# Kernel optimization log

Measured on AMD Instinct MI355X. Metric: run time of the kernel, lower is better.

The kernel has to match this reference:

```python
import jax, jax.numpy as jnp
import numpy as np

B, F, S, P, E, H = 64, 32, 512, 96, 8, 2048
TOP_K = 2
ALPHA = 10.0
ENT_EPS = 1e-8
CV_EPS = 1e-10


def setup_inputs() -> dict:
    key = jax.random.key(0)
    ks = jax.random.split(key, 8)
    s = 0.02
    return {
        "x": jax.random.normal(ks[0], (B, F, S), dtype=jnp.float32),
        "time_embedding": jax.random.normal(ks[1], (B, F, S), dtype=jnp.float32),
        "Wg": jax.random.normal(ks[2], (S, E), dtype=jnp.float32) * s,
        "bg": jnp.zeros((E,), dtype=jnp.float32),
        "W1": jax.random.normal(ks[3], (E, S, H), dtype=jnp.float32) * s,
        "b1": jnp.zeros((E, H), dtype=jnp.float32),
        "W2": jax.random.normal(ks[4], (E, H, P), dtype=jnp.float32) * s,
        "b2": jnp.zeros((E, P), dtype=jnp.float32),
    }


def _gates(tf, Wg, bg):
    # tf: [F, B, S] -> logits [F, B, E]
    logits = jnp.einsum('fbs,se->fbe', tf, Wg) + bg
    # kthvalue(x, E - top_k + 1) = (E - top_k)-th entry (0-based) of ascending sort = k-th largest
    kth = jnp.sort(logits, axis=-1)[..., E - TOP_K]  # [F, B]
    mask = logits < kth[..., None]
    sm = jax.nn.softmax(logits, axis=-1)
    dec = jnp.where(mask, ALPHA * jnp.log(sm + 1.0), ALPHA * (jnp.exp(sm) - 1.0))
    return jax.nn.softmax(dec, axis=-1)  # [F, B, E]


def reference(x, time_embedding, Wg, bg, W1, b1, W2, b2):
    xf = jnp.transpose(x, (1, 0, 2))               # [F, B, S]
    tf = jnp.transpose(time_embedding, (1, 0, 2))  # [F, B, S]
    gates = _gates(tf, Wg, bg)                     # [F, B, E]

    # all experts on all features (eval mode: dropout = identity)
    h = jax.nn.gelu(jnp.einsum('fbs,esh->febh', xf, W1) + b1[None, :, None, :], approximate=False)
    eo = jnp.einsum('febh,ehp->febp', h, W2) + b2[None, :, None, :]  # [F, E, B, P]
    out = jnp.einsum('fbe,febp->fbp', gates, eo)   # gated weighted sum
    output = jnp.transpose(out, (1, 0, 2))         # [B, F, P]

    # selector loss: cv_squared of importance = gates.sum(batch) expanded over pred_len
    gsum = gates.sum(axis=1)                       # [F, E]
    imp = jnp.broadcast_to(gsum[..., None], (F, E, P)).reshape(F, E * P)
    cv = jnp.var(imp, axis=1, ddof=1) / (jnp.mean(imp, axis=1) ** 2 + CV_EPS)
    selector_loss = jnp.sum(cv)                    # loss_coef = 1.0

    # entropy loss: importance1 = gates.mean(batch) expanded over pred_len
    gmean = gates.mean(axis=1)                     # [F, E]
    imp1 = jnp.broadcast_to(gmean[..., None], (F, E, P))
    entropy_loss = jnp.sum((-imp1 * jnp.log(imp1 + ENT_EPS)).mean(axis=(1, 2)))

    return output, selector_loss, entropy_loss
```

## Files before the change

### kernel.cpp

```cpp
#include <hip/hip_runtime.h>
#include <math.h>

#define B_ 64
#define F_ 32
#define S_ 512
#define P_ 96
#define E_ 8
#define H_ 2048
#define M_ 2048

#define BM 128
#define BH 128
#define BK 64
#define HGROUPS 4
#define HPG (H_ / HGROUPS)
#define NHC (HPG / BH)
#define NKC (S_ / BK)

#define XPITCH 72
#define W1PITCH 72
#define HPITCH 136
#define W2PITCH 136

typedef __bf16 bf16x8 __attribute__((ext_vector_type(8)));
typedef float f32x4 __attribute__((ext_vector_type(4)));
typedef unsigned int u32x4 __attribute__((ext_vector_type(4)));
typedef unsigned int u32x2 __attribute__((ext_vector_type(2)));

#define MFMA16(a, b, c) __builtin_amdgcn_mfma_f32_16x16x32_bf16((a), (b), (c), 0, 0, 0)

__device__ __forceinline__ unsigned short f2bf(float f) {
  unsigned int u = __float_as_uint(f);
  return (unsigned short)((u + 0x7FFFu + ((u >> 16) & 1u)) >> 16);
}

__global__ __launch_bounds__(256) void k_convert_x(const float* __restrict__ x,
                                                   unsigned short* __restrict__ xbf) {
  int i = (blockIdx.x * 256 + threadIdx.x) * 4;
  f32x4 v = *(const f32x4*)(x + i);
  unsigned int lo = (unsigned int)f2bf(v[0]) | ((unsigned int)f2bf(v[1]) << 16);
  unsigned int hi = (unsigned int)f2bf(v[2]) | ((unsigned int)f2bf(v[3]) << 16);
  u32x2 o = {lo, hi};
  *(u32x2*)(xbf + i) = o;
}

template <int R, int C>
__global__ __launch_bounds__(256) void k_transpose(const float* __restrict__ in,
                                                   unsigned short* __restrict__ outbf) {
  __shared__ float tile[32][33];
  int e = blockIdx.z;
  const float* src = in + (size_t)e * R * C;
  unsigned short* dst = outbf + (size_t)e * R * C;
  int c0 = blockIdx.x * 32, r0 = blockIdx.y * 32;
  int tx = threadIdx.x & 31, ty = threadIdx.x >> 5;
#pragma unroll
  for (int i = 0; i < 4; ++i) {
    int r = ty * 4 + i;
    tile[r][tx] = src[(size_t)(r0 + r) * C + c0 + tx];
  }
  __syncthreads();
#pragma unroll
  for (int i = 0; i < 4; ++i) {
    int c = ty * 4 + i;
    dst[(size_t)(c0 + c) * R + r0 + tx] = f2bf(tile[tx][c]);
  }
}

__global__ __launch_bounds__(256) void k_gates(const float* __restrict__ te,
                                               const float* __restrict__ Wg,
                                               const float* __restrict__ bg,
                                               float* __restrict__ gates) {
  int wave = threadIdx.x >> 6;
  int lane = threadIdx.x & 63;
  int m = blockIdx.x * 4 + wave;
  const float* trow = te + (size_t)m * S_;
  float acc[E_];
#pragma unroll
  for (int e = 0; e < E_; ++e) acc[e] = 0.f;
  for (int s = lane; s < S_; s += 64) {
    float t = trow[s];
    const f32x4* wgr = (const f32x4*)(Wg + s * E_);
    f32x4 a = wgr[0], b = wgr[1];
    acc[0] += t * a[0]; acc[1] += t * a[1]; acc[2] += t * a[2]; acc[3] += t * a[3];
    acc[4] += t * b[0]; acc[5] += t * b[1]; acc[6] += t * b[2]; acc[7] += t * b[3];
  }
#pragma unroll
  for (int e = 0; e < E_; ++e) {
#pragma unroll
    for (int off = 32; off > 0; off >>= 1) acc[e] += __shfl_xor(acc[e], off, 64);
  }
  if (lane == 0) {
    float lg[E_];
    float m1 = -3.4e38f, m2 = -3.4e38f;
#pragma unroll
    for (int e = 0; e < E_; ++e) {
      float v = acc[e] + bg[e];
      lg[e] = v;
      if (v > m1) { m2 = m1; m1 = v; }
      else if (v > m2) { m2 = v; }
    }
    float den = 0.f, sm[E_];
#pragma unroll
    for (int e = 0; e < E_; ++e) { sm[e] = expf(lg[e] - m1); den += sm[e]; }
    float inv = 1.f / den;
    float dmax = -3.4e38f, dec[E_];
#pragma unroll
    for (int e = 0; e < E_; ++e) {
      float p = sm[e] * inv;
      float d = (lg[e] < m2) ? (10.f * logf(p + 1.f)) : (10.f * (expf(p) - 1.f));
      dec[e] = d;
      dmax = fmaxf(dmax, d);
    }
    float dden = 0.f;
#pragma unroll
    for (int e = 0; e < E_; ++e) { dec[e] = expf(dec[e] - dmax); dden += dec[e]; }
    float dinv = 1.f / dden;
#pragma unroll
    for (int e = 0; e < E_; ++e) gates[m * E_ + e] = dec[e] * dinv;
  }
}

__global__ __launch_bounds__(256) void k_loss(const float* __restrict__ gates,
                                              float* __restrict__ lout) {
  __shared__ float gsum[F_][E_];
  __shared__ float cvs[F_], ents[F_];
  int t = threadIdx.x;
  int f = t >> 3, e = t & 7;
  float s = 0.f;
  for (int b = 0; b < B_; ++b) s += gates[(size_t)(b * F_ + f) * E_ + e];
  gsum[f][e] = s;
  __syncthreads();
  if (t < F_) {
    float mean = 0.f;
#pragma unroll
    for (int k = 0; k < E_; ++k) mean += gsum[t][k];
    mean *= (1.f / E_);
    float ss = 0.f;
#pragma unroll
    for (int k = 0; k < E_; ++k) { float d = gsum[t][k] - mean; ss += d * d; }
    float var = (float)P_ * ss / (float)(E_ * P_ - 1);
    cvs[t] = var / (mean * mean + 1e-10f);
    float ent = 0.f;
#pragma unroll
    for (int k = 0; k < E_; ++k) { float g = gsum[t][k] * (1.f / B_); ent += -g * logf(g + 1e-8f); }
    ents[t] = ent * (1.f / E_);
  }
  __syncthreads();
  if (t == 0) {
    float a = 0.f, b = 0.f;
    for (int k = 0; k < F_; ++k) { a += cvs[k]; b += ents[k]; }
    lout[0] = a;
    lout[1] = b;
  }
}

__global__ __launch_bounds__(256, 2) void k_experts(
    const unsigned short* __restrict__ xbf,
    const unsigned short* __restrict__ w1t,
    const unsigned short* __restrict__ w2t,
    const float* __restrict__ b1,
    const float* __restrict__ b2,
    const float* __restrict__ gates,
    float* __restrict__ out)
{
  __shared__ __align__(16) unsigned short Xks[BM * XPITCH];
  __shared__ __align__(16) unsigned short Hs[BM * HPITCH];
  __shared__ __align__(16) unsigned short Ws[P_ * W2PITCH];

  const int tid = threadIdx.x;
  const int wave = tid >> 6, lane = tid & 63;
  const int l15 = lane & 15, quad = lane >> 4;
  const int e = blockIdx.x;
  const int m0 = blockIdx.y * BM;
  const int hbase = blockIdx.z * HPG;

  const unsigned short* __restrict__ w1e = w1t + ((size_t)e * H_ + hbase) * S_;
  const unsigned short* __restrict__ w2e = w2t + (size_t)e * P_ * H_ + hbase;
  const float* __restrict__ b1e = b1 + e * H_ + hbase;

  const int rw = (wave >> 1) * 64;
  const int cw = (wave & 1) * 64;

  const int srow = tid >> 3;
  const int scol = (tid & 7) * 8;
  const int trow = tid >> 4;
  const int tcol = (tid & 15) * 8;

  const f32x4 fz = {0.f, 0.f, 0.f, 0.f};
  f32x4 acc2[2][6];
#pragma unroll
  for (int rt = 0; rt < 2; ++rt)
#pragma unroll
    for (int j = 0; j < 6; ++j) acc2[rt][j] = fz;

  for (int hc = 0; hc < NHC; ++hc) {
    f32x4 acc1[4][4];
#pragma unroll
    for (int i = 0; i < 4; ++i)
#pragma unroll
      for (int j = 0; j < 4; ++j) acc1[i][j] = fz;

    u32x4 xreg[4], w1reg[4];
#pragma unroll
    for (int p = 0; p < 4; ++p) {
      int rr = p * 32 + srow;
      xreg[p]  = *(const u32x4*)(xbf + (size_t)(m0 + rr) * S_ + scol);
      w1reg[p] = *(const u32x4*)(w1e + (size_t)(hc * BH + rr) * S_ + scol);
    }
    for (int kc = 0; kc < NKC; ++kc) {
      __syncthreads();
#pragma unroll
      for (int p = 0; p < 4; ++p) {
        int rr = p * 32 + srow;
        *(u32x4*)&Xks[rr * XPITCH + scol] = xreg[p];
        *(u32x4*)&Ws[rr * W1PITCH + scol] = w1reg[p];
      }
      __syncthreads();
      if (kc + 1 < NKC) {
#pragma unroll
        for (int p = 0; p < 4; ++p) {
          int rr = p * 32 + srow;
          xreg[p]  = *(const u32x4*)(xbf + (size_t)(m0 + rr) * S_ + (kc + 1) * BK + scol);
          w1reg[p] = *(const u32x4*)(w1e + (size_t)(hc * BH + rr) * S_ + (kc + 1) * BK + scol);
        }
      }
#pragma unroll
      for (int kk = 0; kk < 2; ++kk) {
        bf16x8 af[4], bfr[4];
#pragma unroll
        for (int i = 0; i < 4; ++i)
          af[i] = *(const bf16x8*)&Xks[(rw + i * 16 + l15) * XPITCH + kk * 32 + quad * 8];
#pragma unroll
        for (int j = 0; j < 4; ++j)
          bfr[j] = *(const bf16x8*)&Ws[(cw + j * 16 + l15) * W1PITCH + kk * 32 + quad * 8];
#pragma unroll
        for (int i = 0; i < 4; ++i)
#pragma unroll
          for (int j = 0; j < 4; ++j)
            acc1[i][j] = MFMA16(af[i], bfr[j], acc1[i][j]);
      }
    }
    u32x4 w2reg[6];
#pragma unroll
    for (int p = 0; p < 6; ++p) {
      int rr = p * 16 + trow;
      w2reg[p] = *(const u32x4*)(w2e + (size_t)rr * H_ + hc * BH + tcol);
    }
#pragma unroll
    for (int j = 0; j < 4; ++j) {
      int n = hc * BH + cw + j * 16 + l15;
      float bias = b1e[n];
#pragma unroll
      for (int i = 0; i < 4; ++i) {
#pragma unroll
        for (int r = 0; r < 4; ++r) {
          float xv = acc1[i][j][r] + bias;
          float g = 0.5f * xv * (1.0f + erff(xv * 0.70710678118654752f));
          Hs[(rw + i * 16 + quad * 4 + r) * HPITCH + cw + j * 16 + l15] = f2bf(g);
        }
      }
    }
    __syncthreads();
#pragma unroll
    for (int p = 0; p < 6; ++p) {
      int rr = p * 16 + trow;
      *(u32x4*)&Ws[rr * W2PITCH + tcol] = w2reg[p];
    }
    __syncthreads();
#pragma unroll
    for (int kk = 0; kk < 4; ++kk) {
      bf16x8 a0 = *(const bf16x8*)&Hs[(wave * 32 + l15) * HPITCH + kk * 32 + quad * 8];
      bf16x8 a1 = *(const bf16x8*)&Hs[(wave * 32 + 16 + l15) * HPITCH + kk * 32 + quad * 8];
#pragma unroll
      for (int j = 0; j < 6; ++j) {
        bf16x8 b = *(const bf16x8*)&Ws[(j * 16 + l15) * W2PITCH + kk * 32 + quad * 8];
        acc2[0][j] = MFMA16(a0, b, acc2[0][j]);
        acc2[1][j] = MFMA16(a1, b, acc2[1][j]);
      }
    }
  }
#pragma unroll
  for (int rt = 0; rt < 2; ++rt) {
#pragma unroll
    for (int r = 0; r < 4; ++r) {
      int m = m0 + wave * 32 + rt * 16 + quad * 4 + r;
      float g = gates[m * E_ + e];
#pragma unroll
      for (int j = 0; j < 6; ++j) {
        int col = j * 16 + l15;
        float v = acc2[rt][j][r];
        if (blockIdx.z == 0) v += b2[e * P_ + col];
        atomicAdd(&out[(size_t)m * P_ + col], g * v);
      }
    }
  }
}

extern "C" void kernel_launch(void* const* d_in, const int* in_sizes, int n_in,
                              void* d_out, int out_size, void* d_ws, size_t ws_size,
                              hipStream_t stream) {
  const float* x  = (const float*)d_in[0];
  const float* te = (const float*)d_in[1];
  const float* Wg = (const float*)d_in[2];
  const float* bg = (const float*)d_in[3];
  const float* W1 = (const float*)d_in[4];
  const float* b1 = (const float*)d_in[5];
  const float* W2 = (const float*)d_in[6];
  const float* b2 = (const float*)d_in[7];
  float* out = (float*)d_out;

  char* ws = (char*)d_ws;
  float* gates        = (float*)ws;
  unsigned short* xbf = (unsigned short*)(ws + 65536);
  unsigned short* w1t = (unsigned short*)(ws + 65536 + 2097152);
  unsigned short* w2t = (unsigned short*)(ws + 65536 + 2097152 + 16777216);

  hipMemsetAsync(d_out, 0, (size_t)out_size * sizeof(float), stream);
  k_convert_x<<<(M_ * S_) / 1024, 256, 0, stream>>>(x, xbf);
  k_transpose<S_, H_><<<dim3(H_ / 32, S_ / 32, E_), 256, 0, stream>>>(W1, w1t);
  k_transpose<H_, P_><<<dim3(P_ / 32, H_ / 32, E_), 256, 0, stream>>>(W2, w2t);
  k_gates<<<M_ / 4, 256, 0, stream>>>(te, Wg, bg, gates);
  k_loss<<<1, 256, 0, stream>>>(gates, out + (size_t)M_ * P_);
  k_experts<<<dim3(E_, M_ / BM, HGROUPS), 256, 0, stream>>>(xbf, w1t, w2t, b1, b2, gates, out);
}
```

Baseline: 203.8 us.

## Fuse prep kernels, fold loss into experts, double-buffer W1 and read X/W2 from global

Merges the x conversion, both weight transposes and the gate computation into one k_prep launch, and moves the loss reduction into an extra z-slice of the expert kernel, cutting the launch count from six to two plus the memset. Inside the expert GEMM, W1 tiles are double-buffered in LDS with one barrier per k-step, while X and W2 fragments are loaded straight from global memory into registers. Exact erf GELU is replaced by a sigmoid-based approximation built on exp2 and rcp intrinsics, and the H store is vectorized. The GELU approximation changes numerics and could exceed tolerance. The direct global fragment loads depend on cache hits for their latency.

New measurement: 269.5 us. 32.2% more time.

```diff
diff --git a/kernel.cpp b/kernel.cpp
--- a/kernel.cpp
+++ b/kernel.cpp
@@ -17,62 +17,90 @@
 #define NHC (HPG / BH)
 #define NKC (S_ / BK)
 
-#define XPITCH 72
 #define W1PITCH 72
-#define HPITCH 136
-#define W2PITCH 136
+#define HPITCH 132
 
 typedef __bf16 bf16x8 __attribute__((ext_vector_type(8)));
+typedef __bf16 bf16x4 __attribute__((ext_vector_type(4)));
 typedef float f32x4 __attribute__((ext_vector_type(4)));
 typedef unsigned int u32x4 __attribute__((ext_vector_type(4)));
-typedef unsigned int u32x2 __attribute__((ext_vector_type(2)));
 
 #define MFMA16(a, b, c) __builtin_amdgcn_mfma_f32_16x16x32_bf16((a), (b), (c), 0, 0, 0)
 
-__device__ __forceinline__ unsigned short f2bf(float f) {
-  unsigned int u = __float_as_uint(f);
-  return (unsigned short)((u + 0x7FFFu + ((u >> 16) & 1u)) >> 16);
-}
-
-__global__ __launch_bounds__(256) void k_convert_x(const float* __restrict__ x,
-                                                   unsigned short* __restrict__ xbf) {
-  int i = (blockIdx.x * 256 + threadIdx.x) * 4;
-  f32x4 v = *(const f32x4*)(x + i);
-  unsigned int lo = (unsigned int)f2bf(v[0]) | ((unsigned int)f2bf(v[1]) << 16);
-  unsigned int hi = (unsigned int)f2bf(v[2]) | ((unsigned int)f2bf(v[3]) << 16);
-  u32x2 o = {lo, hi};
-  *(u32x2*)(xbf + i) = o;
-}
-
-template <int R, int C>
-__global__ __launch_bounds__(256) void k_transpose(const float* __restrict__ in,
-                                                   unsigned short* __restrict__ outbf) {
-  __shared__ float tile[32][33];
-  int e = blockIdx.z;
-  const float* src = in + (size_t)e * R * C;
-  unsigned short* dst = outbf + (size_t)e * R * C;
-  int c0 = blockIdx.x * 32, r0 = blockIdx.y * 32;
-  int tx = threadIdx.x & 31, ty = threadIdx.x >> 5;
-#pragma unroll
-  for (int i = 0; i < 4; ++i) {
-    int r = ty * 4 + i;
-    tile[r][tx] = src[(size_t)(r0 + r) * C + c0 + tx];
+__device__ __forceinline__ float fast_gelu(float x) {
+  float e = __builtin_amdgcn_exp2f(-2.45546696f * x);
+  return x * __builtin_amdgcn_rcpf(1.0f + e);
+}
+
+#define PREP_GRID 4096
+
+__device__ __forceinline__ void transpose_tile(const float* __restrict__ src,
+                                               __bf16* __restrict__ dst,
+                                               int R, int C, int r0, int c0, int cw,
+                                               float* tile ) {
+  const int tid = threadIdx.x;
+  {
+    int row = tid >> 2;
+    int cseg = (tid & 3) * 16;
+    const float* s = src + (size_t)(r0 + row) * C + c0;
+#pragma unroll
+    for (int k = 0; k < 4; ++k) {
+      int c = cseg + k * 4;
+      if (c < cw) *(f32x4*)&tile[row * 68 + c] = *(const f32x4*)(s + c);
+    }
   }
   __syncthreads();
-#pragma unroll
-  for (int i = 0; i < 4; ++i) {
-    int c = ty * 4 + i;
-    dst[(size_t)(c0 + c) * R + r0 + tx] = f2bf(tile[tx][c]);
-  }
-}
-
-__global__ __launch_bounds__(256) void k_gates(const float* __restrict__ te,
-                                               const float* __restrict__ Wg,
-                                               const float* __restrict__ bg,
-                                               float* __restrict__ gates) {
-  int wave = threadIdx.x >> 6;
-  int lane = threadIdx.x & 63;
-  int m = blockIdx.x * 4 + wave;
+  {
+    int r = tid & 63, cg = tid >> 6;
+#pragma unroll
+    for (int k = 0; k < 16; ++k) {
+      int c = cg * 16 + k;
+      if (c < cw) dst[(size_t)(c0 + c) * R + r0 + r] = (__bf16)tile[r * 68 + c];
+    }
+  }
+}
+
+__global__ __launch_bounds__(256) void k_prep(const float* __restrict__ x,
+                                              const float* __restrict__ te,
+                                              const float* __restrict__ Wg,
+                                              const float* __restrict__ bg,
+                                              const float* __restrict__ W1,
+                                              const float* __restrict__ W2,
+                                              __bf16* __restrict__ xbf,
+                                              __bf16* __restrict__ w1t,
+                                              __bf16* __restrict__ w2t,
+                                              float* __restrict__ gates) {
+  __shared__ float tile[64 * 68];
+  const int blk = blockIdx.x;
+  const int tid = threadIdx.x;
+
+  if (blk < 2048) {
+    int e = blk >> 8, tt = blk & 255;
+    int r0 = (tt >> 5) * 64;
+    int c0 = (tt & 31) * 64;
+    transpose_tile(W1 + (size_t)e * S_ * H_, w1t + (size_t)e * H_ * S_,
+                   S_, H_, r0, c0, 64, tile);
+    return;
+  }
+  if (blk < 2560) {
+    int tt = blk - 2048;
+    int e = tt >> 6, u = tt & 63;
+    int r0 = (u >> 1) * 64;
+    int c0 = (u & 1) * 64;
+    int cw = (c0 == 0) ? 64 : 32;
+    transpose_tile(W2 + (size_t)e * H_ * P_, w2t + (size_t)e * P_ * H_,
+                   H_, P_, r0, c0, cw, tile);
+    return;
+  }
+  if (blk < 3584) {
+    size_t i = (size_t)(blk - 2560) * 1024 + (size_t)tid * 4;
+    f32x4 v = *(const f32x4*)(x + i);
+    bf16x4 o = {(__bf16)v[0], (__bf16)v[1], (__bf16)v[2], (__bf16)v[3]};
+    *(bf16x4*)(xbf + i) = o;
+    return;
+  }
+  int wave = tid >> 6, lane = tid & 63;
+  int m = (blk - 3584) * 4 + wave;
   const float* trow = te + (size_t)m * S_;
   float acc[E_];
 #pragma unroll
@@ -120,71 +148,75 @@
   }
 }
 
-__global__ __launch_bounds__(256) void k_loss(const float* __restrict__ gates,
-                                              float* __restrict__ lout) {
-  __shared__ float gsum[F_][E_];
-  __shared__ float cvs[F_], ents[F_];
-  int t = threadIdx.x;
-  int f = t >> 3, e = t & 7;
-  float s = 0.f;
-  for (int b = 0; b < B_; ++b) s += gates[(size_t)(b * F_ + f) * E_ + e];
-  gsum[f][e] = s;
-  __syncthreads();
-  if (t < F_) {
-    float mean = 0.f;
-#pragma unroll
-    for (int k = 0; k < E_; ++k) mean += gsum[t][k];
-    mean *= (1.f / E_);
-    float ss = 0.f;
-#pragma unroll
-    for (int k = 0; k < E_; ++k) { float d = gsum[t][k] - mean; ss += d * d; }
-    float var = (float)P_ * ss / (float)(E_ * P_ - 1);
-    cvs[t] = var / (mean * mean + 1e-10f);
-    float ent = 0.f;
-#pragma unroll
-    for (int k = 0; k < E_; ++k) { float g = gsum[t][k] * (1.f / B_); ent += -g * logf(g + 1e-8f); }
-    ents[t] = ent * (1.f / E_);
-  }
-  __syncthreads();
-  if (t == 0) {
-    float a = 0.f, b = 0.f;
-    for (int k = 0; k < F_; ++k) { a += cvs[k]; b += ents[k]; }
-    lout[0] = a;
-    lout[1] = b;
-  }
-}
-
 __global__ __launch_bounds__(256, 2) void k_experts(
-    const unsigned short* __restrict__ xbf,
-    const unsigned short* __restrict__ w1t,
-    const unsigned short* __restrict__ w2t,
+    const __bf16* __restrict__ xbf,
+    const __bf16* __restrict__ w1t,
+    const __bf16* __restrict__ w2t,
     const float* __restrict__ b1,
     const float* __restrict__ b2,
     const float* __restrict__ gates,
     float* __restrict__ out)
 {
-  __shared__ __align__(16) unsigned short Xks[BM * XPITCH];
-  __shared__ __align__(16) unsigned short Hs[BM * HPITCH];
-  __shared__ __align__(16) unsigned short Ws[P_ * W2PITCH];
+  __shared__ __align__(16) __bf16 W1s[2][BM * W1PITCH];
+  __shared__ __align__(16) __bf16 Hs[BM * HPITCH];
 
   const int tid = threadIdx.x;
+
+  if (blockIdx.z == HGROUPS) {
+    if (blockIdx.x != 0 || blockIdx.y != 0) return;
+    float* gsum = (float*)&W1s[0][0];
+    float* cvs  = gsum + F_ * E_;
+    float* ents = cvs + F_;
+    int f = tid >> 3, e = tid & 7;
+    float s = 0.f;
+    for (int b = 0; b < B_; ++b) s += gates[(size_t)(b * F_ + f) * E_ + e];
+    gsum[f * E_ + e] = s;
+    __syncthreads();
+    if (tid < F_) {
+      float mean = 0.f;
+#pragma unroll
+      for (int k = 0; k < E_; ++k) mean += gsum[tid * E_ + k];
+      mean *= (1.f / E_);
+      float ss = 0.f;
+#pragma unroll
+      for (int k = 0; k < E_; ++k) { float d = gsum[tid * E_ + k] - mean; ss += d * d; }
+      float var = (float)P_ * ss / (float)(E_ * P_ - 1);
+      cvs[tid] = var / (mean * mean + 1e-10f);
+      float ent = 0.f;
+#pragma unroll
+      for (int k = 0; k < E_; ++k) { float g = gsum[tid * E_ + k] * (1.f / B_); ent += -g * logf(g + 1e-8f); }
+      ents[tid] = ent * (1.f / E_);
+    }
+    __syncthreads();
+    if (tid == 0) {
+      float a = 0.f, b = 0.f;
+      for (int k = 0; k < F_; ++k) { a += cvs[k]; b += ents[k]; }
+      out[(size_t)M_ * P_ + 0] = a;
+      out[(size_t)M_ * P_ + 1] = b;
+    }
+    return;
+  }
+
   const int wave = tid >> 6, lane = tid & 63;
   const int l15 = lane & 15, quad = lane >> 4;
   const int e = blockIdx.x;
   const int m0 = blockIdx.y * BM;
   const int hbase = blockIdx.z * HPG;
 
-  const unsigned short* __restrict__ w1e = w1t + ((size_t)e * H_ + hbase) * S_;
-  const unsigned short* __restrict__ w2e = w2t + (size_t)e * P_ * H_ + hbase;
+  const __bf16* __restrict__ w1e = w1t + ((size_t)e * H_ + hbase) * S_;
+  const __bf16* __restrict__ w2e = w2t + (size_t)e * P_ * H_ + hbase;
   const float* __restrict__ b1e = b1 + e * H_ + hbase;
 
-  const int rw = (wave >> 1) * 64;
-  const int cw = (wave & 1) * 64;
+  const int hh = (wave >> 1) * 64;
+  const int mm = (wave & 1) * 64;
 
   const int srow = tid >> 3;
   const int scol = (tid & 7) * 8;
-  const int trow = tid >> 4;
-  const int tcol = (tid & 15) * 8;
+
+  const __bf16* xrow[4];
+#pragma unroll
+  for (int j = 0; j < 4; ++j)
+    xrow[j] = xbf + (size_t)(m0 + mm + j * 16 + l15) * S_ + quad * 8;
 
   const f32x4 fz = {0.f, 0.f, 0.f, 0.f};
   f32x4 acc2[2][6];
@@ -193,97 +225,87 @@
 #pragma unroll
     for (int j = 0; j < 6; ++j) acc2[rt][j] = fz;
 
+  const int w32 = wave * 32;
+
   for (int hc = 0; hc < NHC; ++hc) {
+    const __bf16* __restrict__ w1hc = w1e + (size_t)(hc * BH) * S_;
     f32x4 acc1[4][4];
 #pragma unroll
     for (int i = 0; i < 4; ++i)
 #pragma unroll
       for (int j = 0; j < 4; ++j) acc1[i][j] = fz;
 
-    u32x4 xreg[4], w1reg[4];
-#pragma unroll
-    for (int p = 0; p < 4; ++p) {
-      int rr = p * 32 + srow;
-      xreg[p]  = *(const u32x4*)(xbf + (size_t)(m0 + rr) * S_ + scol);
-      w1reg[p] = *(const u32x4*)(w1e + (size_t)(hc * BH + rr) * S_ + scol);
-    }
+    u32x4 w1reg[4];
+#pragma unroll
+    for (int p = 0; p < 4; ++p)
+      w1reg[p] = *(const u32x4*)(w1hc + (size_t)(p * 32 + srow) * S_ + scol);
+#pragma unroll
+    for (int p = 0; p < 4; ++p)
+      *(u32x4*)&W1s[0][(p * 32 + srow) * W1PITCH + scol] = w1reg[p];
+    __syncthreads();
+
     for (int kc = 0; kc < NKC; ++kc) {
+      if (kc + 1 < NKC) {
+#pragma unroll
+        for (int p = 0; p < 4; ++p)
+          w1reg[p] = *(const u32x4*)(w1hc + (size_t)(p * 32 + srow) * S_ + (kc + 1) * BK + scol);
+      }
+      const __bf16* wbuf = W1s[kc & 1];
+#pragma unroll
+      for (int kk = 0; kk < 2; ++kk) {
+        bf16x8 a[4], b[4];
+#pragma unroll
+        for (int j = 0; j < 4; ++j)
+          b[j] = *(const bf16x8*)(xrow[j] + kc * BK + kk * 32);
+#pragma unroll
+        for (int i = 0; i < 4; ++i)
+          a[i] = *(const bf16x8*)&wbuf[(hh + i * 16 + l15) * W1PITCH + kk * 32 + quad * 8];
+#pragma unroll
+        for (int i = 0; i < 4; ++i)
+#pragma unroll
+          for (int j = 0; j < 4; ++j)
+            acc1[i][j] = MFMA16(a[i], b[j], acc1[i][j]);
+      }
+      if (kc + 1 < NKC) {
+#pragma unroll
+        for (int p = 0; p < 4; ++p)
+          *(u32x4*)&W1s[(kc + 1) & 1][(p * 32 + srow) * W1PITCH + scol] = w1reg[p];
+      }
       __syncthreads();
-#pragma unroll
-      for (int p = 0; p < 4; ++p) {
-        int rr = p * 32 + srow;
-        *(u32x4*)&Xks[rr * XPITCH + scol] = xreg[p];
-        *(u32x4*)&Ws[rr * W1PITCH + scol] = w1reg[p];
-      }
-      __syncthreads();
-      if (kc + 1 < NKC) {
-#pragma unroll
-        for (int p = 0; p < 4; ++p) {
-          int rr = p * 32 + srow;
-          xreg[p]  = *(const u32x4*)(xbf + (size_t)(m0 + rr) * S_ + (kc + 1) * BK + scol);
-          w1reg[p] = *(const u32x4*)(w1e + (size_t)(hc * BH + rr) * S_ + (kc + 1) * BK + scol);
-        }
-      }
-#pragma unroll
-      for (int kk = 0; kk < 2; ++kk) {
-        bf16x8 af[4], bfr[4];
-#pragma unroll
-        for (int i = 0; i < 4; ++i)
-          af[i] = *(const bf16x8*)&Xks[(rw + i * 16 + l15) * XPITCH + kk * 32 + quad * 8];
-#pragma unroll
-        for (int j = 0; j < 4; ++j)
-          bfr[j] = *(const bf16x8*)&Ws[(cw + j * 16 + l15) * W1PITCH + kk * 32 + quad * 8];
-#pragma unroll
-        for (int i = 0; i < 4; ++i)
-#pragma unroll
-          for (int j = 0; j < 4; ++j)
-            acc1[i][j] = MFMA16(af[i], bfr[j], acc1[i][j]);
-      }
-    }
-    u32x4 w2reg[6];
-#pragma unroll
-    for (int p = 0; p < 6; ++p) {
-      int rr = p * 16 + trow;
-      w2reg[p] = *(const u32x4*)(w2e + (size_t)rr * H_ + hc * BH + tcol);
-    }
-#pragma unroll
-    for (int j = 0; j < 4; ++j) {
-      int n = hc * BH + cw + j * 16 + l15;
-      float bias = b1e[n];
-#pragma unroll
-      for (int i = 0; i < 4; ++i) {
-#pragma unroll
-        for (int r = 0; r < 4; ++r) {
-          float xv = acc1[i][j][r] + bias;
-          float g = 0.5f * xv * (1.0f + erff(xv * 0.70710678118654752f));
-          Hs[(rw + i * 16 + quad * 4 + r) * HPITCH + cw + j * 16 + l15] = f2bf(g);
-        }
+    }
+
+#pragma unroll
+    for (int i = 0; i < 4; ++i) {
+      f32x4 bv = *(const f32x4*)&b1e[hc * BH + hh + i * 16 + quad * 4];
+#pragma unroll
+      for (int j = 0; j < 4; ++j) {
+        bf16x4 hv;
+#pragma unroll
+        for (int r = 0; r < 4; ++r)
+          hv[r] = (__bf16)fast_gelu(acc1[i][j][r] + bv[r]);
+        *(bf16x4*)&Hs[(mm + j * 16 + l15) * HPITCH + hh + i * 16 + quad * 4] = hv;
       }
     }
     __syncthreads();
-#pragma unroll
-    for (int p = 0; p < 6; ++p) {
-      int rr = p * 16 + trow;
-      *(u32x4*)&Ws[rr * W2PITCH + tcol] = w2reg[p];
-    }
-    __syncthreads();
+
 #pragma unroll
     for (int kk = 0; kk < 4; ++kk) {
-      bf16x8 a0 = *(const bf16x8*)&Hs[(wave * 32 + l15) * HPITCH + kk * 32 + quad * 8];
-      bf16x8 a1 = *(const bf16x8*)&Hs[(wave * 32 + 16 + l15) * HPITCH + kk * 32 + quad * 8];
+      bf16x8 a0 = *(const bf16x8*)&Hs[(w32 + l15) * HPITCH + kk * 32 + quad * 8];
+      bf16x8 a1 = *(const bf16x8*)&Hs[(w32 + 16 + l15) * HPITCH + kk * 32 + quad * 8];
 #pragma unroll
       for (int j = 0; j < 6; ++j) {
-        bf16x8 b = *(const bf16x8*)&Ws[(j * 16 + l15) * W2PITCH + kk * 32 + quad * 8];
+        bf16x8 b = *(const bf16x8*)(w2e + (size_t)(j * 16 + l15) * H_ + hc * BH + kk * 32 + quad * 8);
         acc2[0][j] = MFMA16(a0, b, acc2[0][j]);
         acc2[1][j] = MFMA16(a1, b, acc2[1][j]);
       }
     }
   }
+
 #pragma unroll
   for (int rt = 0; rt < 2; ++rt) {
 #pragma unroll
     for (int r = 0; r < 4; ++r) {
-      int m = m0 + wave * 32 + rt * 16 + quad * 4 + r;
+      int m = m0 + w32 + rt * 16 + quad * 4 + r;
       float g = gates[m * E_ + e];
 #pragma unroll
       for (int j = 0; j < 6; ++j) {
@@ -310,16 +332,12 @@
   float* out = (float*)d_out;
 
   char* ws = (char*)d_ws;
-  float* gates        = (float*)ws;
-  unsigned short* xbf = (unsigned short*)(ws + 65536);
-  unsigned short* w1t = (unsigned short*)(ws + 65536 + 2097152);
-  unsigned short* w2t = (unsigned short*)(ws + 65536 + 2097152 + 16777216);
+  float* gates = (float*)ws;
+  __bf16* xbf  = (__bf16*)(ws + 65536);
+  __bf16* w1t  = (__bf16*)(ws + 65536 + 2097152);
+  __bf16* w2t  = (__bf16*)(ws + 65536 + 2097152 + 16777216);
 
   hipMemsetAsync(d_out, 0, (size_t)out_size * sizeof(float), stream);
-  k_convert_x<<<(M_ * S_) / 1024, 256, 0, stream>>>(x, xbf);
-  k_transpose<S_, H_><<<dim3(H_ / 32, S_ / 32, E_), 256, 0, stream>>>(W1, w1t);
-  k_transpose<H_, P_><<<dim3(P_ / 32, H_ / 32, E_), 256, 0, stream>>>(W2, w2t);
-  k_gates<<<M_ / 4, 256, 0, stream>>>(te, Wg, bg, gates);
-  k_loss<<<1, 256, 0, stream>>>(gates, out + (size_t)M_ * P_);
-  k_experts<<<dim3(E_, M_ / BM, HGROUPS), 256, 0, stream>>>(xbf, w1t, w2t, b1, b2, gates, out);
-}
+  k_prep<<<PREP_GRID, 256, 0, stream>>>(x, te, Wg, bg, W1, W2, xbf, w1t, w2t, gates);
+  k_experts<<<dim3(E_, M_ / BM, HGROUPS + 1), 256, 0, stream>>>(xbf, w1t, w2t, b1, b2, gates, out);
+}
```
